# Performance work log

Measured on AMD Instinct MI355X. Metric: run time of the kernel, lower is better.

The kernel has to match this reference:

```python
import jax, jax.numpy as jnp
import numpy as np

B, C, H, W = 4, 64, 160, 160
O = 64
G = 4            # offset groups
KH = KW = 3
K = KH * KW
STRIDE, PAD = 1, 1


def setup_inputs() -> dict:
    key = jax.random.key(0)
    k1, k2, k3, k4, k5 = jax.random.split(key, 5)
    return {
        "warp_ref": jax.random.normal(k1, (B, C, H, W), jnp.float32),
        "offset_map": jax.random.normal(k2, (B, 2 * G * K, H, W), jnp.float32),
        "w_reg": jax.random.normal(k3, (O, C, KH, KW), jnp.float32) * 0.05,
        "w_mod": jax.random.normal(k4, (G * K, C, KH, KW), jnp.float32) * 0.05,
        "b_mod": jax.random.normal(k5, (G * K,), jnp.float32) * 0.05,
    }


def _conv2d(x, w, b):
    y = jax.lax.conv_general_dilated(x, w, (STRIDE, STRIDE), [(PAD, PAD), (PAD, PAD)],
                                     dimension_numbers=("NCHW", "OIHW", "NCHW"))
    return y + b[None, :, None, None]


def _deform_conv2d(x, offset, mask, weight):
    # Modulated deformable conv (DCNv2), torchvision semantics.
    b, c, h, w = x.shape
    ho, wo = h, w  # stride=1, pad=1, 3x3 -> same spatial size
    cg = c // G
    # offset layout: [B, 2*G*K, Ho, Wo] -> (group, kpos, (y, x))
    off = offset.reshape(b, G, K, 2, ho, wo)
    oy, ox = off[:, :, :, 0], off[:, :, :, 1]              # [B,G,K,Ho,Wo]
    ki, kj = jnp.meshgrid(jnp.arange(KH), jnp.arange(KW), indexing="ij")
    ki = ki.reshape(K).astype(x.dtype)
    kj = kj.reshape(K).astype(x.dtype)
    base_y = jnp.arange(ho, dtype=x.dtype) * STRIDE - PAD
    base_x = jnp.arange(wo, dtype=x.dtype) * STRIDE - PAD
    # absolute sampling positions [B,G,K,Ho,Wo]
    py = oy + base_y[None, None, None, :, None] + ki[None, None, :, None, None]
    px = ox + base_x[None, None, None, None, :] + kj[None, None, :, None, None]
    y0 = jnp.floor(py)
    x0 = jnp.floor(px)
    wy = py - y0
    wx = px - x0
    xg = x.reshape(b, G, cg, h * w)
    # gather per (batch, offset-group): xf [Cg, H*W], ix [K,Ho,Wo] -> [Cg,K,Ho,Wo]
    gather = jax.vmap(jax.vmap(lambda xf, ix: xf[:, ix]))

    def corner(yc, xc, cw):
        valid = (yc >= 0) & (yc < h) & (xc >= 0) & (xc < w)   # zero padding outside
        yi = jnp.clip(yc, 0, h - 1).astype(jnp.int32)
        xi = jnp.clip(xc, 0, w - 1).astype(jnp.int32)
        g = gather(xg, yi * w + xi)                            # [B,G,Cg,K,Ho,Wo]
        return g * (cw * valid.astype(x.dtype))[:, :, None]

    sampled = (corner(y0, x0, (1 - wy) * (1 - wx))
               + corner(y0, x0 + 1, (1 - wy) * wx)
               + corner(y0 + 1, x0, wy * (1 - wx))
               + corner(y0 + 1, x0 + 1, wy * wx))              # [B,G,Cg,K,Ho,Wo]
    wr = weight.reshape(weight.shape[0], G, cg, K)             # [O,G,Cg,K]
    m = mask.reshape(b, G, K, ho, wo)                          # modulation mask
    return jnp.einsum("ogck,bgckhw,bgkhw->bohw", wr, sampled, m)


def reference(warp_ref, offset_map, w_reg, w_mod, b_mod):
    h, w = warp_ref.shape[2], warp_ref.shape[3]
    offset_range = min(h, w) * 0.5 / 2
    off = offset_range * 2.0 * jax.nn.sigmoid(offset_map) - offset_range
    modulator = 2.0 * jax.nn.sigmoid(_conv2d(warp_ref, w_mod, b_mod))
    out = _deform_conv2d(warp_ref, off, modulator, w_reg)
    return out, off
```

## Files before the change

kernel.cpp:

```cpp
#include <hip/hip_runtime.h>

#define B_    4
#define C_    64
#define H_    160
#define W_    160
#define O_    64
#define G_    4
#define K_    9
#define CG_   16
#define MODC_ 36
#define OFFC_ 72
#define HW_   (H_*W_)

typedef __attribute__((ext_vector_type(8))) short short8;
typedef __attribute__((ext_vector_type(4))) float f32x4;

#define NCHUNK_ 18

__device__ __forceinline__ float sigmoidf(float v) {
    return 1.0f / (1.0f + __expf(-v));
}

__device__ __forceinline__ short f2bf(float f) {
    unsigned u = __float_as_uint(f);
    u += 0x7FFFu + ((u >> 16) & 1u);
    return (short)(u >> 16);
}

__device__ __forceinline__ float bf2f(short s) {
    return __uint_as_float(((unsigned)(unsigned short)s) << 16);
}

__global__ __launch_bounds__(256) void k_prep(const float* __restrict__ x,
                                              const float* __restrict__ omap,
                                              const float* __restrict__ wreg,
                                              const float* __restrict__ wmod,
                                              unsigned short* __restrict__ xt,
                                              short* __restrict__ wA_def,
                                              short* __restrict__ wA_mod,
                                              float* __restrict__ out_off) {
    int blk = blockIdx.x;
    if (blk < 1600) {
        __shared__ unsigned short lds[256][17];
        int bg   = blk / 100;
        int pix0 = (blk % 100) * 256;
        const float* src = x + (size_t)bg * CG_ * HW_ + pix0;
#pragma unroll
        for (int c = 0; c < CG_; ++c)
            lds[threadIdx.x][c] = (unsigned short)f2bf(src[c * HW_ + threadIdx.x]);
        __syncthreads();
        unsigned w[8];
#pragma unroll
        for (int q = 0; q < 8; ++q)
            w[q] = (unsigned)lds[threadIdx.x][2 * q] |
                   ((unsigned)lds[threadIdx.x][2 * q + 1] << 16);
        uint4* dst = (uint4*)(xt + ((size_t)bg * HW_ + pix0 + threadIdx.x) * CG_);
        dst[0] = make_uint4(w[0], w[1], w[2], w[3]);
        dst[1] = make_uint4(w[4], w[5], w[6], w[7]);
    } else if (blk < 8800) {
        int i = (blk - 1600) * 256 + threadIdx.x;
        float4 v = ((const float4*)omap)[i];
        float4 r;
        r.x = 80.0f * sigmoidf(v.x) - 40.0f;
        r.y = 80.0f * sigmoidf(v.y) - 40.0f;
        r.z = 80.0f * sigmoidf(v.z) - 40.0f;
        r.w = 80.0f * sigmoidf(v.w) - 40.0f;
        ((float4*)out_off)[i] = r;
    } else {
        int tid = (blk - 8800) * 256 + threadIdx.x;
        if (tid < NCHUNK_ * 4 * 64) {
            int lane = tid & 63;
            int mt   = (tid >> 6) & 3;
            int cc   = tid >> 8;
            int quad = lane >> 4;
            int o    = mt * 16 + (lane & 15);
#pragma unroll
            for (int j = 0; j < 8; ++j) {
                int idx = cc * 32 + quad * 8 + j;
                int gk = idx >> 4, c = idx & 15;
                int g = gk / 9, kk = gk - g * 9;
                wA_def[(size_t)tid * 8 + j] = f2bf(wreg[((o * C_) + g * CG_ + c) * K_ + kk]);
            }
        } else {
            int t2 = tid - NCHUNK_ * 4 * 64;
            if (t2 < NCHUNK_ * 3 * 64) {
                int lane = t2 & 63;
                int mt   = (t2 >> 6) % 3;
                int cc   = t2 / 192;
                int quad = lane >> 4;
                int jch  = mt * 16 + (lane & 15);
#pragma unroll
                for (int j = 0; j < 8; ++j) {
                    int idx = cc * 32 + quad * 8 + j;
                    int t = idx >> 6, c = idx & 63;
                    float v = (jch < MODC_) ? wmod[((jch * C_) + c) * K_ + t] : 0.0f;
                    wA_mod[(size_t)t2 * 8 + j] = f2bf(v);
                }
            }
        }
    }
}

__global__ __launch_bounds__(256, 4) void k_fused(const unsigned short* __restrict__ xt,
                                                  const float* __restrict__ out_off,
                                                  const short* __restrict__ wA_mod,
                                                  const short* __restrict__ wA_def,
                                                  const float* __restrict__ bm,
                                                  float* __restrict__ out) {
    __shared__ float modl[4][MODC_][16];
    int b    = (blockIdx.x & 7) >> 1;
    int tile = ((blockIdx.x >> 3) << 1) + (blockIdx.x & 1);
    int wave = threadIdx.x >> 6;
    int lane = threadIdx.x & 63;
    int quad = lane >> 4;
    int px   = lane & 15;
    int p    = tile * 64 + wave * 16 + px;
    int y    = p / W_;
    int x    = p - y * W_;

    f32x4 m0 = {}, m1 = {}, m2 = {};
    const short8* wm = (const short8*)wA_mod;

#pragma unroll 6
    for (int cc = 0; cc < NCHUNK_; ++cc) {
        int t  = cc >> 1;
        int dy = t / 3 - 1;
        int dx = t - (t / 3) * 3 - 1;
        int yy = y + dy, xx = x + dx;
        bool ok = (((unsigned)yy < (unsigned)H_) && ((unsigned)xx < (unsigned)W_));
        int yc = min(max(yy, 0), H_ - 1);
        int xc = min(max(xx, 0), W_ - 1);
        int ch0 = (cc & 1) * 32 + quad * 8;
        int g   = ch0 >> 4;
        int cl  = ch0 & 15;
        int4 raw = *(const int4*)(xt + ((size_t)(b * G_ + g) * HW_ +
                                        (size_t)(yc * W_ + xc)) * CG_ + cl);
        if (!ok) raw = make_int4(0, 0, 0, 0);
        short8 bfr = *(short8*)&raw;

        const short8* w = wm + cc * 192;
        m0 = __builtin_amdgcn_mfma_f32_16x16x32_bf16(w[lane],       bfr, m0, 0, 0, 0);
        m1 = __builtin_amdgcn_mfma_f32_16x16x32_bf16(w[64 + lane],  bfr, m1, 0, 0, 0);
        m2 = __builtin_amdgcn_mfma_f32_16x16x32_bf16(w[128 + lane], bfr, m2, 0, 0, 0);
    }

    float* ml = &modl[wave][0][0];
#pragma unroll
    for (int reg = 0; reg < 4; ++reg) {
        int j0 = quad * 4 + reg;
        ml[j0 * 16 + px]        = 2.0f * sigmoidf(m0[reg] + bm[j0]);
        ml[(16 + j0) * 16 + px] = 2.0f * sigmoidf(m1[reg] + bm[16 + j0]);
        if (32 + j0 < MODC_)
            ml[(32 + j0) * 16 + px] = 2.0f * sigmoidf(m2[reg] + bm[32 + j0]);
    }
    __syncthreads();

    f32x4 acc0 = {}, acc1 = {}, acc2 = {}, acc3 = {};
    const float* offp = out_off + (size_t)b * OFFC_ * HW_ + p;
    const short8* wa  = (const short8*)wA_def;
    int cbase = (quad & 1) * 8;

#pragma unroll 1
    for (int sc = 0; sc < 3; ++sc) {
        float oyv[6], oxv[6], fmv[6];
#pragma unroll
        for (int u = 0; u < 6; ++u) {
            int cc = sc * 6 + u;
            int gk = cc * 2 + (quad >> 1);
            int g  = gk / 9;
            int kk = gk - g * 9;
            oyv[u] = offp[(size_t)(g * 18 + kk * 2) * HW_];
            oxv[u] = offp[(size_t)(g * 18 + kk * 2 + 1) * HW_];
            fmv[u] = ml[gk * 16 + px];
        }
#pragma unroll
        for (int u = 0; u < 6; ++u) {
            int cc = sc * 6 + u;
            int gk = cc * 2 + (quad >> 1);
            int g  = gk / 9;
            int kk = gk - g * 9;
            int ki = kk / 3;
            int kj = kk - ki * 3;

            float py  = oyv[u] + (float)(y - 1 + ki);
            float pxf = oxv[u] + (float)(x - 1 + kj);
            float y0f = floorf(py), x0f = floorf(pxf);
            float wy  = py - y0f,   wx  = pxf - x0f;
            int y0 = (int)y0f, x0i = (int)x0f;
            int y1 = y0 + 1,   x1  = x0i + 1;
            float vy0 = ((unsigned)y0  < (unsigned)H_) ? 1.0f : 0.0f;
            float vy1 = ((unsigned)y1  < (unsigned)H_) ? 1.0f : 0.0f;
            float vx0 = ((unsigned)x0i < (unsigned)W_) ? 1.0f : 0.0f;
            float vx1 = ((unsigned)x1  < (unsigned)W_) ? 1.0f : 0.0f;
            int yc0 = min(max(y0, 0), H_ - 1);
            int yc1 = min(max(y1, 0), H_ - 1);
            int xc0 = min(max(x0i, 0), W_ - 1);
            int xc1 = min(max(x1, 0), W_ - 1);

            float fm  = fmv[u];
            float w00 = (1.0f - wy) * (1.0f - wx) * vy0 * vx0 * fm;
            float w01 = (1.0f - wy) * wx          * vy0 * vx1 * fm;
            float w10 = wy          * (1.0f - wx) * vy1 * vx0 * fm;
            float w11 = wy          * wx          * vy1 * vx1 * fm;

            const unsigned short* xg = xt + ((size_t)(b * G_ + g) * HW_) * CG_ + cbase;
            short8 s00 = *(const short8*)(xg + (size_t)(yc0 * W_ + xc0) * CG_);
            short8 s01 = *(const short8*)(xg + (size_t)(yc0 * W_ + xc1) * CG_);
            short8 s10 = *(const short8*)(xg + (size_t)(yc1 * W_ + xc0) * CG_);
            short8 s11 = *(const short8*)(xg + (size_t)(yc1 * W_ + xc1) * CG_);

            short8 bfr;
#pragma unroll
            for (int i = 0; i < 8; ++i) {
                float v = fmaf(w00, bf2f(s00[i]),
                          fmaf(w01, bf2f(s01[i]),
                          fmaf(w10, bf2f(s10[i]), w11 * bf2f(s11[i]))));
                bfr[i] = f2bf(v);
            }

            const short8* w = wa + cc * 256;
            acc0 = __builtin_amdgcn_mfma_f32_16x16x32_bf16(w[lane],       bfr, acc0, 0, 0, 0);
            acc1 = __builtin_amdgcn_mfma_f32_16x16x32_bf16(w[64 + lane],  bfr, acc1, 0, 0, 0);
            acc2 = __builtin_amdgcn_mfma_f32_16x16x32_bf16(w[128 + lane], bfr, acc2, 0, 0, 0);
            acc3 = __builtin_amdgcn_mfma_f32_16x16x32_bf16(w[192 + lane], bfr, acc3, 0, 0, 0);
        }
    }

    float* op = out + (size_t)b * O_ * HW_ + p;
#pragma unroll
    for (int reg = 0; reg < 4; ++reg) {
        int o0 = quad * 4 + reg;
        op[(size_t)o0 * HW_]        = acc0[reg];
        op[(size_t)(16 + o0) * HW_] = acc1[reg];
        op[(size_t)(32 + o0) * HW_] = acc2[reg];
        op[(size_t)(48 + o0) * HW_] = acc3[reg];
    }
}

extern "C" void kernel_launch(void* const* d_in, const int* in_sizes, int n_in,
                              void* d_out, int out_size, void* d_ws, size_t ws_size,
                              hipStream_t stream) {
    const float* warp = (const float*)d_in[0];
    const float* omap = (const float*)d_in[1];
    const float* wreg = (const float*)d_in[2];
    const float* wmod = (const float*)d_in[3];
    const float* bmod = (const float*)d_in[4];

    float* out     = (float*)d_out;
    float* out_off = out + (size_t)B_ * O_ * HW_;

    unsigned short* xt = (unsigned short*)d_ws;
    short* wA_def = (short*)(xt + (size_t)B_ * C_ * HW_);
    short* wA_mod = wA_def + NCHUNK_ * 4 * 64 * 8;

    hipLaunchKernelGGL(k_prep, dim3(8832), dim3(256), 0, stream,
                       warp, omap, wreg, wmod, xt, wA_def, wA_mod, out_off);
    hipLaunchKernelGGL(k_fused, dim3(1600), dim3(256), 0, stream,
                       xt, out_off, wA_mod, wA_def, bmod, out);
}
```

Measured before the change: 202.5 us.

## Software-pipeline deformable gathers and use packed bf16 bilinear combine

Restructures the deformable sampling loop so the four corner gathers and bilinear weights for the next chunk are issued before the MFMAs of the current chunk consume the previous one. All offset loads are hoisted up front. The bilinear interpolation now uses packed two-wide float math with a cheaper round-half-up bf16 pack. The block-wide barrier is dropped because each wave reads only its own LDS slice. This aims to hide gather latency and cut VALU work. It raises register pressure under the existing launch bounds, which risks spills, and slightly changes rounding.

```diff
diff --git a/kernel.cpp b/kernel.cpp
--- a/kernel.cpp
+++ b/kernel.cpp
@@ -14,6 +14,7 @@
 
 typedef __attribute__((ext_vector_type(8))) short short8;
 typedef __attribute__((ext_vector_type(4))) float f32x4;
+typedef __attribute__((ext_vector_type(2))) float f32x2;
 
 #define NCHUNK_ 18
 
@@ -27,8 +28,28 @@
     return (short)(u >> 16);
 }
 
-__device__ __forceinline__ float bf2f(short s) {
-    return __uint_as_float(((unsigned)(unsigned short)s) << 16);
+__device__ __forceinline__ f32x2 unpk(unsigned u) {
+    f32x2 r;
+    r.x = __uint_as_float(u << 16);
+    r.y = __uint_as_float(u & 0xffff0000u);
+    return r;
+}
+
+__device__ __forceinline__ unsigned pack2(float a, float b) {
+    unsigned ua = __float_as_uint(a) + 0x8000u;
+    unsigned ub = __float_as_uint(b) + 0x8000u;
+#if __has_builtin(__builtin_amdgcn_perm)
+    return __builtin_amdgcn_perm(ub, ua, 0x07060302u);
+#else
+    return (ua >> 16) | (ub & 0xffff0000u);
+#endif
+}
+
+__device__ __forceinline__ unsigned comb2(int a, int b, int c, int d,
+                                          f32x2 w0, f32x2 w1, f32x2 w2, f32x2 w3) {
+    f32x2 v = w0 * unpk((unsigned)a) + w1 * unpk((unsigned)b)
+            + w2 * unpk((unsigned)c) + w3 * unpk((unsigned)d);
+    return pack2(v.x, v.y);
 }
 
 __global__ __launch_bounds__(256) void k_prep(const float* __restrict__ x,
@@ -101,6 +122,59 @@
     }
 }
 
+
+#define PREPB(cc_, par_) do {                                                  \
+    int gk = (cc_) * 2 + qh;                                                   \
+    int g  = gk / 9, kk = gk - g * 9;                                          \
+    int ki = kk / 3, kj = kk - ki * 3;                                         \
+    float fm = ml[gk * 16 + px];                                               \
+    float py  = oy[cc_] + (float)(y - 1 + ki);                                 \
+    float pxf = ox[cc_] + (float)(x - 1 + kj);                                 \
+    float y0f = floorf(py), x0f = floorf(pxf);                                 \
+    float wy = py - y0f, wx = pxf - x0f;                                       \
+    int y0 = (int)y0f, x0i = (int)x0f;                                         \
+    int y1 = y0 + 1, x1 = x0i + 1;                                             \
+    float vy0 = ((unsigned)y0  < (unsigned)H_) ? 1.0f : 0.0f;                  \
+    float vy1 = ((unsigned)y1  < (unsigned)H_) ? 1.0f : 0.0f;                  \
+    float vx0 = ((unsigned)x0i < (unsigned)W_) ? 1.0f : 0.0f;                  \
+    float vx1 = ((unsigned)x1  < (unsigned)W_) ? 1.0f : 0.0f;                  \
+    int yc0 = min(max(y0, 0), H_ - 1);                                         \
+    int yc1 = min(max(y1, 0), H_ - 1);                                         \
+    int xc0 = min(max(x0i, 0), W_ - 1);                                        \
+    int xc1 = min(max(x1, 0), W_ - 1);                                         \
+    cw[par_][0] = (1.0f - wy) * (1.0f - wx) * vy0 * vx0 * fm;                  \
+    cw[par_][1] = (1.0f - wy) * wx          * vy0 * vx1 * fm;                  \
+    cw[par_][2] = wy * (1.0f - wx) * vy1 * vx0 * fm;                           \
+    cw[par_][3] = wy * wx          * vy1 * vx1 * fm;                           \
+    const unsigned short* xg = xt + ((size_t)(b * G_ + g) * HW_) * CG_ + cbase;\
+    G[par_][0] = *(const int4*)(xg + (size_t)(yc0 * W_ + xc0) * CG_);          \
+    G[par_][1] = *(const int4*)(xg + (size_t)(yc0 * W_ + xc1) * CG_);          \
+    G[par_][2] = *(const int4*)(xg + (size_t)(yc1 * W_ + xc0) * CG_);          \
+    G[par_][3] = *(const int4*)(xg + (size_t)(yc1 * W_ + xc1) * CG_);          \
+} while (0)
+
+#define CONSB(cc_, par_) do {                                                  \
+    f32x2 w0 = {cw[par_][0], cw[par_][0]};                                     \
+    f32x2 w1 = {cw[par_][1], cw[par_][1]};                                     \
+    f32x2 w2 = {cw[par_][2], cw[par_][2]};                                     \
+    f32x2 w3 = {cw[par_][3], cw[par_][3]};                                     \
+    int4 bi;                                                                   \
+    bi.x = (int)comb2(G[par_][0].x, G[par_][1].x, G[par_][2].x, G[par_][3].x,  \
+                      w0, w1, w2, w3);                                         \
+    bi.y = (int)comb2(G[par_][0].y, G[par_][1].y, G[par_][2].y, G[par_][3].y,  \
+                      w0, w1, w2, w3);                                         \
+    bi.z = (int)comb2(G[par_][0].z, G[par_][1].z, G[par_][2].z, G[par_][3].z,  \
+                      w0, w1, w2, w3);                                         \
+    bi.w = (int)comb2(G[par_][0].w, G[par_][1].w, G[par_][2].w, G[par_][3].w,  \
+                      w0, w1, w2, w3);                                         \
+    short8 bfr = *(short8*)&bi;                                                \
+    const short8* wp = wa + (cc_) * 256;                                       \
+    acc0 = __builtin_amdgcn_mfma_f32_16x16x32_bf16(wp[lane],       bfr, acc0, 0, 0, 0); \
+    acc1 = __builtin_amdgcn_mfma_f32_16x16x32_bf16(wp[64 + lane],  bfr, acc1, 0, 0, 0); \
+    acc2 = __builtin_amdgcn_mfma_f32_16x16x32_bf16(wp[128 + lane], bfr, acc2, 0, 0, 0); \
+    acc3 = __builtin_amdgcn_mfma_f32_16x16x32_bf16(wp[192 + lane], bfr, acc3, 0, 0, 0); \
+} while (0)
+
 __global__ __launch_bounds__(256, 4) void k_fused(const unsigned short* __restrict__ xt,
                                                   const float* __restrict__ out_off,
                                                   const short* __restrict__ wA_mod,
@@ -121,7 +195,7 @@
     f32x4 m0 = {}, m1 = {}, m2 = {};
     const short8* wm = (const short8*)wA_mod;
 
-#pragma unroll 6
+#pragma unroll
     for (int cc = 0; cc < NCHUNK_; ++cc) {
         int t  = cc >> 1;
         int dy = t / 3 - 1;
@@ -130,7 +204,7 @@
         bool ok = (((unsigned)yy < (unsigned)H_) && ((unsigned)xx < (unsigned)W_));
         int yc = min(max(yy, 0), H_ - 1);
         int xc = min(max(xx, 0), W_ - 1);
-        int ch0 = (cc & 1) * 32 + quad * 8;
+        int ch0 = (cc & 1) * 32 + (quad << 3);
         int g   = ch0 >> 4;
         int cl  = ch0 & 15;
         int4 raw = *(const int4*)(xt + ((size_t)(b * G_ + g) * HW_ +
@@ -153,78 +227,32 @@
         if (32 + j0 < MODC_)
             ml[(32 + j0) * 16 + px] = 2.0f * sigmoidf(m2[reg] + bm[32 + j0]);
     }
-    __syncthreads();
 
     f32x4 acc0 = {}, acc1 = {}, acc2 = {}, acc3 = {};
     const float* offp = out_off + (size_t)b * OFFC_ * HW_ + p;
     const short8* wa  = (const short8*)wA_def;
+    int qh    = quad >> 1;
     int cbase = (quad & 1) * 8;
 
-#pragma unroll 1
-    for (int sc = 0; sc < 3; ++sc) {
-        float oyv[6], oxv[6], fmv[6];
-#pragma unroll
-        for (int u = 0; u < 6; ++u) {
-            int cc = sc * 6 + u;
-            int gk = cc * 2 + (quad >> 1);
-            int g  = gk / 9;
-            int kk = gk - g * 9;
-            oyv[u] = offp[(size_t)(g * 18 + kk * 2) * HW_];
-            oxv[u] = offp[(size_t)(g * 18 + kk * 2 + 1) * HW_];
-            fmv[u] = ml[gk * 16 + px];
-        }
-#pragma unroll
-        for (int u = 0; u < 6; ++u) {
-            int cc = sc * 6 + u;
-            int gk = cc * 2 + (quad >> 1);
-            int g  = gk / 9;
-            int kk = gk - g * 9;
-            int ki = kk / 3;
-            int kj = kk - ki * 3;
-
-            float py  = oyv[u] + (float)(y - 1 + ki);
-            float pxf = oxv[u] + (float)(x - 1 + kj);
-            float y0f = floorf(py), x0f = floorf(pxf);
-            float wy  = py - y0f,   wx  = pxf - x0f;
-            int y0 = (int)y0f, x0i = (int)x0f;
-            int y1 = y0 + 1,   x1  = x0i + 1;
-            float vy0 = ((unsigned)y0  < (unsigned)H_) ? 1.0f : 0.0f;
-            float vy1 = ((unsigned)y1  < (unsigned)H_) ? 1.0f : 0.0f;
-            float vx0 = ((unsigned)x0i < (unsigned)W_) ? 1.0f : 0.0f;
-            float vx1 = ((unsigned)x1  < (unsigned)W_) ? 1.0f : 0.0f;
-            int yc0 = min(max(y0, 0), H_ - 1);
-            int yc1 = min(max(y1, 0), H_ - 1);
-            int xc0 = min(max(x0i, 0), W_ - 1);
-            int xc1 = min(max(x1, 0), W_ - 1);
-
-            float fm  = fmv[u];
-            float w00 = (1.0f - wy) * (1.0f - wx) * vy0 * vx0 * fm;
-            float w01 = (1.0f - wy) * wx          * vy0 * vx1 * fm;
-            float w10 = wy          * (1.0f - wx) * vy1 * vx0 * fm;
-            float w11 = wy          * wx          * vy1 * vx1 * fm;
-
-            const unsigned short* xg = xt + ((size_t)(b * G_ + g) * HW_) * CG_ + cbase;
-            short8 s00 = *(const short8*)(xg + (size_t)(yc0 * W_ + xc0) * CG_);
-            short8 s01 = *(const short8*)(xg + (size_t)(yc0 * W_ + xc1) * CG_);
-            short8 s10 = *(const short8*)(xg + (size_t)(yc1 * W_ + xc0) * CG_);
-            short8 s11 = *(const short8*)(xg + (size_t)(yc1 * W_ + xc1) * CG_);
-
-            short8 bfr;
-#pragma unroll
-            for (int i = 0; i < 8; ++i) {
-                float v = fmaf(w00, bf2f(s00[i]),
-                          fmaf(w01, bf2f(s01[i]),
-                          fmaf(w10, bf2f(s10[i]), w11 * bf2f(s11[i]))));
-                bfr[i] = f2bf(v);
-            }
-
-            const short8* w = wa + cc * 256;
-            acc0 = __builtin_amdgcn_mfma_f32_16x16x32_bf16(w[lane],       bfr, acc0, 0, 0, 0);
-            acc1 = __builtin_amdgcn_mfma_f32_16x16x32_bf16(w[64 + lane],  bfr, acc1, 0, 0, 0);
-            acc2 = __builtin_amdgcn_mfma_f32_16x16x32_bf16(w[128 + lane], bfr, acc2, 0, 0, 0);
-            acc3 = __builtin_amdgcn_mfma_f32_16x16x32_bf16(w[192 + lane], bfr, acc3, 0, 0, 0);
-        }
-    }
+    float oy[NCHUNK_], ox[NCHUNK_];
+#pragma unroll
+    for (int cc = 0; cc < NCHUNK_; ++cc) {
+        int gk = cc * 2 + qh;
+        int g  = gk / 9, kk = gk - g * 9;
+        oy[cc] = offp[(size_t)(g * 18 + kk * 2) * HW_];
+        ox[cc] = offp[(size_t)(g * 18 + kk * 2 + 1) * HW_];
+    }
+
+    int4  G[2][4];
+    float cw[2][4];
+
+    PREPB(0, 0);
+#pragma unroll
+    for (int cc = 0; cc < NCHUNK_ - 1; ++cc) {
+        PREPB(cc + 1, (cc + 1) & 1);
+        CONSB(cc, cc & 1);
+    }
+    CONSB(NCHUNK_ - 1, (NCHUNK_ - 1) & 1);
 
     float* op = out + (size_t)b * O_ * HW_ + p;
 #pragma unroll
```

New measurement: 189.2 us. -6.6%, faster.
